# Optimization experiments

Hardware: AMD Instinct MI355X
Metric: run time of the kernel (lower is better)

The kernel has to match this reference:

```python
import jax, jax.numpy as jnp
import numpy as np

NUM_ACTIVE = 2  # num_active from init


def setup_inputs() -> dict:
    key = jax.random.key(0)
    k1, k2, k3, k4 = jax.random.split(key, 4)
    B, S, D, H, E = 2, 1024, 1024, 4096, 8
    x = jax.random.normal(k1, (B, S, D), jnp.float32)
    # router initialized to zeros in the torch module, but we use small random
    # weights so routing is non-degenerate for the correctness baseline
    router_w = jax.random.normal(k2, (D, E), jnp.float32) * 0.02
    router_b = jnp.zeros((E,), jnp.float32)
    w12 = jax.random.normal(k3, (E, D, 2 * H), jnp.float32) * (1.0 / np.sqrt(D))
    w3 = jax.random.normal(k4, (E, H, D), jnp.float32) * (1.0 / np.sqrt(H))
    return {"x": x, "router_w": router_w, "router_b": router_b, "w12": w12, "w3": w3}


def reference(x, router_w, router_b, w12, w3):
    E = router_w.shape[-1]
    # router (eval mode: no jitter noise)
    logits = x @ router_w + router_b                      # [B,S,E]
    scores = jax.nn.sigmoid(logits)
    top_s, top_i = jax.lax.top_k(scores, NUM_ACTIVE)      # [B,S,k]
    rw = top_s / (jnp.sum(top_s, axis=-1, keepdims=True) + 1e-6)
    # per-token combine weight for each expert: sum of routed slot weights
    cw = jnp.sum(jax.nn.one_hot(top_i, E, dtype=x.dtype) * rw[..., None], axis=-2)  # [B,S,E]
    # dense all-expert SwiGLU (same math as masked loop in the original)
    x12 = jnp.einsum('bsd,edh->ebsh', x, w12)             # [E,B,S,2H]
    x1, x2 = jnp.split(x12, 2, axis=-1)
    h = jax.nn.silu(x1) * x2                              # [E,B,S,H]
    out = jnp.einsum('ebsh,ehd,bse->bsd', h, w3, cw)      # [B,S,D]
    aux_loss = 0.01 * jnp.mean(logits ** 2)
    return out, aux_loss
```

## Files before the change

### kernel.cpp

```cpp
#include <hip/hip_runtime.h>
#include <hip/hip_bf16.h>

#define TOK 2048
#define DIM 1024
#define HID 4096
#define NE  8

typedef short bf16x8 __attribute__((ext_vector_type(8)));
typedef float f32x4 __attribute__((ext_vector_type(4)));
typedef unsigned short ushort_t;
typedef unsigned int uint_t;

#define SWZB(n) (((((n) >> 2) ^ ((n) >> 4)) & 3) << 4)

__device__ __forceinline__ ushort_t f2bf(float f) {
  uint_t b = __float_as_uint(f);
  uint_t r = (b + 0x7FFFu + ((b >> 16) & 1u)) >> 16;
  return (ushort_t)r;
}
__device__ __forceinline__ float bf2f(ushort_t u) {
  return __uint_as_float(((uint_t)u) << 16);
}
__device__ __forceinline__ uint_t pk2bf(float a, float b) {
  uint_t r;
  asm("v_cvt_pk_bf16_f32 %0, %1, %2" : "=v"(r) : "v"(a), "v"(b));
  return r;
}

__global__ void router_kernel(const float* __restrict__ x,
                              const float* __restrict__ rw,
                              const float* __restrict__ rb,
                              float* __restrict__ tok_ss,
                              int* __restrict__ top_e,
                              float* __restrict__ top_w,
                              ushort_t* __restrict__ xb) {
  const int t = blockIdx.x;
  const int lane = threadIdx.x;
  float acc[NE];
#pragma unroll
  for (int e = 0; e < NE; ++e) acc[e] = 0.f;
  const float4* x4 = (const float4*)(x + (size_t)t * DIM);
  uint2* xb2 = (uint2*)(xb + (size_t)t * DIM);
#pragma unroll
  for (int j = 0; j < 4; ++j) {
    int i = j * 64 + lane;
    float4 v = x4[i];
    uint2 u;
    u.x = pk2bf(v.x, v.y);
    u.y = pk2bf(v.z, v.w);
    xb2[i] = u;
    const float* w = rw + (size_t)i * 4 * NE;
    const float* vp = (const float*)&v;
#pragma unroll
    for (int c = 0; c < 4; ++c)
#pragma unroll
      for (int e = 0; e < NE; ++e) acc[e] += vp[c] * w[c * NE + e];
  }
#pragma unroll
  for (int e = 0; e < NE; ++e) {
    float v = acc[e];
#pragma unroll
    for (int off = 32; off > 0; off >>= 1) v += __shfl_down(v, off, 64);
    acc[e] = v;
  }
  if (lane == 0) {
    float sc[NE];
    float ss = 0.f;
#pragma unroll
    for (int e = 0; e < NE; ++e) {
      float lg = acc[e] + rb[e];
      ss += lg * lg;
      sc[e] = 1.f / (1.f + expf(-lg));
    }
    tok_ss[t] = ss;
    int i0 = 0;
#pragma unroll
    for (int e = 1; e < NE; ++e) if (sc[e] > sc[i0]) i0 = e;
    int i1 = (i0 == 0) ? 1 : 0;
#pragma unroll
    for (int e = 0; e < NE; ++e) if (e != i0 && sc[e] > sc[i1]) i1 = e;
    float s0 = sc[i0], s1 = sc[i1];
    float inv = 1.f / (s0 + s1 + 1e-6f);
    top_e[t * 2 + 0] = i0;
    top_e[t * 2 + 1] = i1;
    top_w[t * 2 + 0] = s0 * inv;
    top_w[t * 2 + 1] = s1 * inv;
  }
}

__global__ void scan_assign_kernel(const int* __restrict__ top_e,
                                   const float* __restrict__ top_w,
                                   int* __restrict__ offsets,
                                   int* __restrict__ list_tok,
                                   float* __restrict__ list_w) {
  __shared__ int lcount[NE];
  __shared__ int loff[NE + 1];
  __shared__ int lfill[NE];
  if (threadIdx.x < NE) lcount[threadIdx.x] = 0;
  __syncthreads();
  for (int i = threadIdx.x; i < TOK * 2; i += 256)
    atomicAdd(&lcount[top_e[i]], 1);
  __syncthreads();
  if (threadIdx.x == 0) {
    int o = 0;
    for (int e = 0; e < NE; ++e) { loff[e] = o; lfill[e] = o; o += lcount[e]; }
    loff[NE] = o;
  }
  __syncthreads();
  if (threadIdx.x <= NE) offsets[threadIdx.x] = loff[threadIdx.x];
  for (int i = threadIdx.x; i < TOK * 2; i += 256) {
    int e = top_e[i];
    int idx = atomicAdd(&lfill[e], 1);
    list_tok[idx] = i >> 1;
    list_w[idx] = top_w[i];
  }
}

__global__ void aux_kernel(const float* __restrict__ tok_ss, float* __restrict__ out_aux) {
  __shared__ float sm[256];
  float s = 0.f;
  for (int t = threadIdx.x; t < TOK; t += 256) s += tok_ss[t];
  sm[threadIdx.x] = s;
  __syncthreads();
  for (int w = 128; w > 0; w >>= 1) {
    if (threadIdx.x < w) sm[threadIdx.x] += sm[threadIdx.x + w];
    __syncthreads();
  }
  if (threadIdx.x == 0) *out_aux = 0.01f * sm[0] / (float)(TOK * NE);
}

__global__ __launch_bounds__(256)
void gemm1_mfma(const ushort_t* __restrict__ xb,
                const float* __restrict__ w12,
                const int* __restrict__ offsets, const int* __restrict__ list_tok,
                ushort_t* __restrict__ hhi) {
  __shared__ __align__(16) ushort_t Ah0[64 * 40];
  __shared__ __align__(16) ushort_t Ah1[64 * 40];
  __shared__ __align__(16) ushort_t B1h0[64 * 40];
  __shared__ __align__(16) ushort_t B1h1[64 * 40];
  __shared__ __align__(16) ushort_t B2h0[64 * 40];
  __shared__ __align__(16) ushort_t B2h1[64 * 40];

  const int e = blockIdx.y >> 5;
  const int rt = blockIdx.y & 31;
  const int rowstart = offsets[e] + rt * 64;
  const int rowend = offsets[e + 1];
  if (rowstart >= rowend) return;
  const int h0 = blockIdx.x * 64;
  const int tid = threadIdx.x;
  const int lane = tid & 63, wid = tid >> 6;
  const int wm = wid >> 1, wn = wid & 1;
  const int lr = lane & 15, kh = lane >> 4;

  f32x4 acc1[2][2], acc2[2][2];
#pragma unroll
  for (int mi = 0; mi < 2; ++mi)
#pragma unroll
    for (int nj = 0; nj < 2; ++nj) {
      acc1[mi][nj] = (f32x4){0.f, 0.f, 0.f, 0.f};
      acc2[mi][nj] = (f32x4){0.f, 0.f, 0.f, 0.f};
    }

  const int arow = tid >> 2, aseg = tid & 3;
  int ar = rowstart + arow;
  int atok = list_tok[ar < rowend ? ar : rowstart];
  const size_t asrc = (size_t)atok * DIM + aseg * 8;
  const int adst = arow * 40 + aseg * 8;

  const int p = tid >> 4, n4 = tid & 15;
  const float* w12e = w12 + (size_t)e * DIM * (2 * HID) + h0 + n4 * 4;
  char* B1c0 = (char*)B1h0;
  char* B1c1 = (char*)B1h1;
  char* B2c0 = (char*)B2h0;
  char* B2c1 = (char*)B2h1;

  int boff[2];
#pragma unroll
  for (int nj = 0; nj < 2; ++nj) {
    int n = wn * 32 + nj * 16 + lr;
    boff[nj] = n * 80 + ((kh * 16) ^ SWZB(n));
  }
  int bwoff[4];
#pragma unroll
  for (int c = 0; c < 4; ++c) {
    int n = n4 * 4 + c;
    bwoff[c] = n * 80 + ((4 * p) ^ SWZB(n));
  }

  uint4 ra0_0, ra1_0, ra0_1, ra1_1;
  float4 w1a0_0, w1b0_0, w2a0_0, w2b0_0, w1a1_0, w1b1_0, w2a1_0, w2b1_0;
  float4 w1a0_1, w1b0_1, w2a0_1, w2b0_1, w1a1_1, w1b1_1, w2a1_1, w2b1_1;

#define G1_LOAD(S, K0) do { \
    ra0_##S = *(const uint4*)&xb[asrc + (K0)]; \
    ra1_##S = *(const uint4*)&xb[asrc + (K0) + 32]; \
    const float* r0 = w12e + (size_t)((K0) + 2 * p) * (2 * HID); \
    w1a0_##S = *(const float4*)r0; \
    w1b0_##S = *(const float4*)(r0 + 2 * HID); \
    w2a0_##S = *(const float4*)(r0 + HID); \
    w2b0_##S = *(const float4*)(r0 + HID + 2 * HID); \
    const float* r1 = w12e + (size_t)((K0) + 32 + 2 * p) * (2 * HID); \
    w1a1_##S = *(const float4*)r1; \
    w1b1_##S = *(const float4*)(r1 + 2 * HID); \
    w2a1_##S = *(const float4*)(r1 + HID); \
    w2b1_##S = *(const float4*)(r1 + HID + 2 * HID); \
  } while (0)

#define G1_STORE(S) do { \
    *(uint4*)&Ah0[adst] = ra0_##S; \
    *(uint4*)&Ah1[adst] = ra1_##S; \
    const float* p1a0 = (const float*)&w1a0_##S; \
    const float* p1b0 = (const float*)&w1b0_##S; \
    const float* p2a0 = (const float*)&w2a0_##S; \
    const float* p2b0 = (const float*)&w2b0_##S; \
    const float* p1a1 = (const float*)&w1a1_##S; \
    const float* p1b1 = (const float*)&w1b1_##S; \
    const float* p2a1 = (const float*)&w2a1_##S; \
    const float* p2b1 = (const float*)&w2b1_##S; \
    _Pragma("unroll") \
    for (int c = 0; c < 4; ++c) { \
      *(uint_t*)(B1c0 + bwoff[c]) = pk2bf(p1a0[c], p1b0[c]); \
      *(uint_t*)(B2c0 + bwoff[c]) = pk2bf(p2a0[c], p2b0[c]); \
      *(uint_t*)(B1c1 + bwoff[c]) = pk2bf(p1a1[c], p1b1[c]); \
      *(uint_t*)(B2c1 + bwoff[c]) = pk2bf(p2a1[c], p2b1[c]); \
    } } while (0)

#define G1_COMPUTE() do { \
    { \
      bf16x8 af[2], b1f[2], b2f[2]; \
      _Pragma("unroll") \
      for (int mi = 0; mi < 2; ++mi) \
        af[mi] = *(bf16x8*)&Ah0[(wm * 32 + mi * 16 + lr) * 40 + kh * 8]; \
      _Pragma("unroll") \
      for (int nj = 0; nj < 2; ++nj) { \
        b1f[nj] = *(bf16x8*)(B1c0 + boff[nj]); \
        b2f[nj] = *(bf16x8*)(B2c0 + boff[nj]); \
      } \
      _Pragma("unroll") \
      for (int mi = 0; mi < 2; ++mi) \
        _Pragma("unroll") \
        for (int nj = 0; nj < 2; ++nj) { \
          acc1[mi][nj] = __builtin_amdgcn_mfma_f32_16x16x32_bf16(af[mi], b1f[nj], acc1[mi][nj], 0, 0, 0); \
          acc2[mi][nj] = __builtin_amdgcn_mfma_f32_16x16x32_bf16(af[mi], b2f[nj], acc2[mi][nj], 0, 0, 0); \
        } \
    } \
    { \
      bf16x8 af[2], b1f[2], b2f[2]; \
      _Pragma("unroll") \
      for (int mi = 0; mi < 2; ++mi) \
        af[mi] = *(bf16x8*)&Ah1[(wm * 32 + mi * 16 + lr) * 40 + kh * 8]; \
      _Pragma("unroll") \
      for (int nj = 0; nj < 2; ++nj) { \
        b1f[nj] = *(bf16x8*)(B1c1 + boff[nj]); \
        b2f[nj] = *(bf16x8*)(B2c1 + boff[nj]); \
      } \
      _Pragma("unroll") \
      for (int mi = 0; mi < 2; ++mi) \
        _Pragma("unroll") \
        for (int nj = 0; nj < 2; ++nj) { \
          acc1[mi][nj] = __builtin_amdgcn_mfma_f32_16x16x32_bf16(af[mi], b1f[nj], acc1[mi][nj], 0, 0, 0); \
          acc2[mi][nj] = __builtin_amdgcn_mfma_f32_16x16x32_bf16(af[mi], b2f[nj], acc2[mi][nj], 0, 0, 0); \
        } \
    } } while (0)

  G1_LOAD(0, 0);
  G1_LOAD(1, 64);
#pragma unroll 1
  for (int k0 = 0; k0 < DIM; k0 += 128) {
    G1_STORE(0);
    __syncthreads();
    if (k0 + 128 < DIM) G1_LOAD(0, k0 + 128);
    G1_COMPUTE();
    __syncthreads();
    G1_STORE(1);
    __syncthreads();
    if (k0 + 192 < DIM) G1_LOAD(1, k0 + 192);
    G1_COMPUTE();
    __syncthreads();
  }
#undef G1_LOAD
#undef G1_STORE
#undef G1_COMPUTE

#pragma unroll
  for (int mi = 0; mi < 2; ++mi)
#pragma unroll
    for (int nj = 0; nj < 2; ++nj)
#pragma unroll
      for (int r = 0; r < 4; ++r) {
        int row_t = wm * 32 + mi * 16 + kh * 4 + r;
        int gr = rowstart + row_t;
        if (gr < rowend) {
          int col = h0 + wn * 32 + nj * 16 + lr;
          float v1 = acc1[mi][nj][r], v2 = acc2[mi][nj][r];
          float hv = (v1 / (1.f + expf(-v1))) * v2;
          hhi[(size_t)gr * HID + col] = f2bf(hv);
        }
      }
}

__global__ __launch_bounds__(256)
void gemm2_mfma(const ushort_t* __restrict__ hhi,
                const float* __restrict__ w3,
                const int* __restrict__ offsets, const float* __restrict__ list_w,
                const int* __restrict__ list_tok,
                float* __restrict__ out) {
  __shared__ __align__(16) ushort_t As0[64 * 40];
  __shared__ __align__(16) ushort_t As1[64 * 40];
  __shared__ __align__(16) ushort_t Bs0[64 * 40];
  __shared__ __align__(16) ushort_t Bs1[64 * 40];

  const int e = blockIdx.y >> 4;
  const int rt = blockIdx.y & 15;
  const int rowstart = offsets[e] + rt * 64;
  const int rowend = offsets[e + 1];
  if (rowstart >= rowend) return;
  const int d0 = blockIdx.x * 64;
  const int tid = threadIdx.x;
  const int lane = tid & 63, wid = tid >> 6;
  const int wm = wid >> 1, wn = wid & 1;
  const int lr = lane & 15, kh = lane >> 4;

  f32x4 acc[2][2];
#pragma unroll
  for (int mi = 0; mi < 2; ++mi)
#pragma unroll
    for (int nj = 0; nj < 2; ++nj) acc[mi][nj] = (f32x4){0.f, 0.f, 0.f, 0.f};

  const int arow = tid >> 2, aseg = tid & 3;
  int gr = rowstart + arow; if (gr >= rowend) gr = rowstart;
  const size_t asrc = (size_t)gr * HID + aseg * 8;
  const int adst = arow * 40 + aseg * 8;

  const int p = tid >> 4, n4 = tid & 15;
  const float* w3e = w3 + (size_t)e * HID * DIM + d0 + n4 * 4;
  char* Bs0c = (char*)Bs0;
  char* Bs1c = (char*)Bs1;

  int boff[2];
#pragma unroll
  for (int nj = 0; nj < 2; ++nj) {
    int n = wn * 32 + nj * 16 + lr;
    boff[nj] = n * 80 + ((kh * 16) ^ SWZB(n));
  }
  int bwoff[4];
#pragma unroll
  for (int c = 0; c < 4; ++c) {
    int n = n4 * 4 + c;
    bwoff[c] = n * 80 + ((4 * p) ^ SWZB(n));
  }

  uint4 ra0_0, ra1_0, ra0_1, ra1_1;
  float4 rb00_0, rb01_0, rb10_0, rb11_0;
  float4 rb00_1, rb01_1, rb10_1, rb11_1;

#define G2_LOAD(S, K0) do { \
    ra0_##S = *(const uint4*)&hhi[asrc + (K0)]; \
    ra1_##S = *(const uint4*)&hhi[asrc + (K0) + 32]; \
    const float* r0 = w3e + (size_t)((K0) + 2 * p) * DIM; \
    rb00_##S = *(const float4*)r0; \
    rb01_##S = *(const float4*)(r0 + DIM); \
    const float* r1 = w3e + (size_t)((K0) + 32 + 2 * p) * DIM; \
    rb10_##S = *(const float4*)r1; \
    rb11_##S = *(const float4*)(r1 + DIM); \
  } while (0)

#define G2_STORE(S) do { \
    *(uint4*)&As0[adst] = ra0_##S; \
    *(uint4*)&As1[adst] = ra1_##S; \
    const float* pv0 = (const float*)&rb00_##S; \
    const float* pv1 = (const float*)&rb01_##S; \
    const float* pw0 = (const float*)&rb10_##S; \
    const float* pw1 = (const float*)&rb11_##S; \
    _Pragma("unroll") \
    for (int c = 0; c < 4; ++c) { \
      *(uint_t*)(Bs0c + bwoff[c]) = pk2bf(pv0[c], pv1[c]); \
      *(uint_t*)(Bs1c + bwoff[c]) = pk2bf(pw0[c], pw1[c]); \
    } } while (0)

#define G2_COMPUTE() do { \
    { \
      bf16x8 af[2], bf[2]; \
      _Pragma("unroll") \
      for (int mi = 0; mi < 2; ++mi) \
        af[mi] = *(bf16x8*)&As0[(wm * 32 + mi * 16 + lr) * 40 + kh * 8]; \
      _Pragma("unroll") \
      for (int nj = 0; nj < 2; ++nj) \
        bf[nj] = *(bf16x8*)(Bs0c + boff[nj]); \
      _Pragma("unroll") \
      for (int mi = 0; mi < 2; ++mi) \
        _Pragma("unroll") \
        for (int nj = 0; nj < 2; ++nj) \
          acc[mi][nj] = __builtin_amdgcn_mfma_f32_16x16x32_bf16(af[mi], bf[nj], acc[mi][nj], 0, 0, 0); \
    } \
    { \
      bf16x8 af[2], bf[2]; \
      _Pragma("unroll") \
      for (int mi = 0; mi < 2; ++mi) \
        af[mi] = *(bf16x8*)&As1[(wm * 32 + mi * 16 + lr) * 40 + kh * 8]; \
      _Pragma("unroll") \
      for (int nj = 0; nj < 2; ++nj) \
        bf[nj] = *(bf16x8*)(Bs1c + boff[nj]); \
      _Pragma("unroll") \
      for (int mi = 0; mi < 2; ++mi) \
        _Pragma("unroll") \
        for (int nj = 0; nj < 2; ++nj) \
          acc[mi][nj] = __builtin_amdgcn_mfma_f32_16x16x32_bf16(af[mi], bf[nj], acc[mi][nj], 0, 0, 0); \
    } } while (0)

  G2_LOAD(0, 0);
  G2_LOAD(1, 64);
#pragma unroll 1
  for (int k0 = 0; k0 < HID; k0 += 128) {
    G2_STORE(0);
    __syncthreads();
    if (k0 + 128 < HID) G2_LOAD(0, k0 + 128);
    G2_COMPUTE();
    __syncthreads();
    G2_STORE(1);
    __syncthreads();
    if (k0 + 192 < HID) G2_LOAD(1, k0 + 192);
    G2_COMPUTE();
    __syncthreads();
  }
#undef G2_LOAD
#undef G2_STORE
#undef G2_COMPUTE

#pragma unroll
  for (int mi = 0; mi < 2; ++mi)
#pragma unroll
    for (int nj = 0; nj < 2; ++nj)
#pragma unroll
      for (int r = 0; r < 4; ++r) {
        int grr = rowstart + wm * 32 + mi * 16 + kh * 4 + r;
        if (grr < rowend) {
          int col = d0 + wn * 32 + nj * 16 + lr;
          int tok = list_tok[grr];
          atomicAdd(&out[(size_t)tok * DIM + col], acc[mi][nj][r] * list_w[grr]);
        }
      }
}

extern "C" void kernel_launch(void* const* d_in, const int* in_sizes, int n_in,
                              void* d_out, int out_size, void* d_ws, size_t ws_size,
                              hipStream_t stream) {
  const float* x   = (const float*)d_in[0];
  const float* rw  = (const float*)d_in[1];
  const float* rb  = (const float*)d_in[2];
  const float* w12 = (const float*)d_in[3];
  const float* w3  = (const float*)d_in[4];
  float* out = (float*)d_out;

  char* ws = (char*)d_ws;
  size_t off = 0;
  auto alloc = [&](size_t bytes) {
    void* p = ws + off;
    off = (off + bytes + 255) & ~255ULL;
    return p;
  };
  int*   offsets  = (int*)alloc((NE + 1) * 4);
  float* tok_ss   = (float*)alloc(TOK * 4);
  int*   top_e    = (int*)alloc(TOK * 2 * 4);
  float* top_w    = (float*)alloc(TOK * 2 * 4);
  int*   list_tok = (int*)alloc(TOK * 2 * 4);
  float* list_w   = (float*)alloc(TOK * 2 * 4);

  ushort_t* xb  = (ushort_t*)alloc((size_t)TOK * DIM * 2);
  ushort_t* hhi = (ushort_t*)alloc((size_t)TOK * 2 * HID * 2);

  hipMemsetAsync(out, 0, (size_t)TOK * DIM * 4, stream);

  hipLaunchKernelGGL(router_kernel, dim3(TOK), dim3(64), 0, stream,
                     x, rw, rb, tok_ss, top_e, top_w, xb);
  hipLaunchKernelGGL(scan_assign_kernel, dim3(1), dim3(256), 0, stream,
                     top_e, top_w, offsets, list_tok, list_w);
  hipLaunchKernelGGL(aux_kernel, dim3(1), dim3(256), 0, stream,
                     tok_ss, out + (size_t)TOK * DIM);

  hipLaunchKernelGGL(gemm1_mfma, dim3(HID / 64, NE * 32), dim3(256), 0, stream,
                     xb, w12, offsets, list_tok, hhi);
  hipLaunchKernelGGL(gemm2_mfma, dim3(DIM / 64, NE * 16), dim3(256), 0, stream,
                     hhi, w3, offsets, list_w, list_tok, out);
}
```

Measured before the change: 364.0 us.

## Load A fragments straight from global into registers and double gemm1 row tile

Both MoE GEMMs stop staging the gathered activation tile in shared memory. Each lane now loads its MFMA A fragments directly from global memory into registers, so only the fp32-to-bf16 weight tile goes through LDS. gemm1 grows its row tile from 64 to 128 tokens per block, which halves how often each block re-reads and converts the fp32 w12 weights, and its K step shrinks to 32 with a single weight buffer. gemm2's grid is widened to 64 row tiles per expert so experts holding more than 1024 routed rows are fully covered; the extra blocks mostly exit early. The trade-off is less-coalesced 16-byte direct global loads, more registers per thread and more barriers per K stride in gemm1.

```diff
diff --git a/kernel.cpp b/kernel.cpp
--- a/kernel.cpp
+++ b/kernel.cpp
@@ -134,16 +134,12 @@
                 const float* __restrict__ w12,
                 const int* __restrict__ offsets, const int* __restrict__ list_tok,
                 ushort_t* __restrict__ hhi) {
-  __shared__ __align__(16) ushort_t Ah0[64 * 40];
-  __shared__ __align__(16) ushort_t Ah1[64 * 40];
-  __shared__ __align__(16) ushort_t B1h0[64 * 40];
-  __shared__ __align__(16) ushort_t B1h1[64 * 40];
-  __shared__ __align__(16) ushort_t B2h0[64 * 40];
-  __shared__ __align__(16) ushort_t B2h1[64 * 40];
+  __shared__ __align__(16) ushort_t B1[64 * 40];
+  __shared__ __align__(16) ushort_t B2[64 * 40];
 
   const int e = blockIdx.y >> 5;
   const int rt = blockIdx.y & 31;
-  const int rowstart = offsets[e] + rt * 64;
+  const int rowstart = offsets[e] + rt * 128;
   const int rowend = offsets[e + 1];
   if (rowstart >= rowend) return;
   const int h0 = blockIdx.x * 64;
@@ -152,27 +148,27 @@
   const int wm = wid >> 1, wn = wid & 1;
   const int lr = lane & 15, kh = lane >> 4;
 
-  f32x4 acc1[2][2], acc2[2][2];
-#pragma unroll
-  for (int mi = 0; mi < 2; ++mi)
+  f32x4 acc1[4][2], acc2[4][2];
+#pragma unroll
+  for (int mi = 0; mi < 4; ++mi)
 #pragma unroll
     for (int nj = 0; nj < 2; ++nj) {
       acc1[mi][nj] = (f32x4){0.f, 0.f, 0.f, 0.f};
       acc2[mi][nj] = (f32x4){0.f, 0.f, 0.f, 0.f};
     }
 
-  const int arow = tid >> 2, aseg = tid & 3;
-  int ar = rowstart + arow;
-  int atok = list_tok[ar < rowend ? ar : rowstart];
-  const size_t asrc = (size_t)atok * DIM + aseg * 8;
-  const int adst = arow * 40 + aseg * 8;
+  const ushort_t* aP[4];
+#pragma unroll
+  for (int mi = 0; mi < 4; ++mi) {
+    int r = rowstart + wm * 64 + mi * 16 + lr;
+    int rr = (r < rowend) ? r : rowstart;
+    aP[mi] = xb + (size_t)list_tok[rr] * DIM + kh * 8;
+  }
 
   const int p = tid >> 4, n4 = tid & 15;
   const float* w12e = w12 + (size_t)e * DIM * (2 * HID) + h0 + n4 * 4;
-  char* B1c0 = (char*)B1h0;
-  char* B1c1 = (char*)B1h1;
-  char* B2c0 = (char*)B2h0;
-  char* B2c1 = (char*)B2h1;
+  char* B1c = (char*)B1;
+  char* B2c = (char*)B2;
 
   int boff[2];
 #pragma unroll
@@ -187,108 +183,79 @@
     bwoff[c] = n * 80 + ((4 * p) ^ SWZB(n));
   }
 
-  uint4 ra0_0, ra1_0, ra0_1, ra1_1;
-  float4 w1a0_0, w1b0_0, w2a0_0, w2b0_0, w1a1_0, w1b1_0, w2a1_0, w2b1_0;
-  float4 w1a0_1, w1b0_1, w2a0_1, w2b0_1, w1a1_1, w1b1_1, w2a1_1, w2b1_1;
-
-#define G1_LOAD(S, K0) do { \
-    ra0_##S = *(const uint4*)&xb[asrc + (K0)]; \
-    ra1_##S = *(const uint4*)&xb[asrc + (K0) + 32]; \
+  bf16x8 a0[4], a1[4];
+  float4 w1a, w1b, w2a, w2b;
+
+#define G1_ALOAD(SET, K0) do { \
+    _Pragma("unroll") \
+    for (int mi = 0; mi < 4; ++mi) SET[mi] = *(const bf16x8*)(aP[mi] + (K0)); \
+  } while (0)
+
+#define G1_BLOAD(K0) do { \
     const float* r0 = w12e + (size_t)((K0) + 2 * p) * (2 * HID); \
-    w1a0_##S = *(const float4*)r0; \
-    w1b0_##S = *(const float4*)(r0 + 2 * HID); \
-    w2a0_##S = *(const float4*)(r0 + HID); \
-    w2b0_##S = *(const float4*)(r0 + HID + 2 * HID); \
-    const float* r1 = w12e + (size_t)((K0) + 32 + 2 * p) * (2 * HID); \
-    w1a1_##S = *(const float4*)r1; \
-    w1b1_##S = *(const float4*)(r1 + 2 * HID); \
-    w2a1_##S = *(const float4*)(r1 + HID); \
-    w2b1_##S = *(const float4*)(r1 + HID + 2 * HID); \
+    w1a = *(const float4*)r0; \
+    w1b = *(const float4*)(r0 + 2 * HID); \
+    w2a = *(const float4*)(r0 + HID); \
+    w2b = *(const float4*)(r0 + HID + 2 * HID); \
   } while (0)
 
-#define G1_STORE(S) do { \
-    *(uint4*)&Ah0[adst] = ra0_##S; \
-    *(uint4*)&Ah1[adst] = ra1_##S; \
-    const float* p1a0 = (const float*)&w1a0_##S; \
-    const float* p1b0 = (const float*)&w1b0_##S; \
-    const float* p2a0 = (const float*)&w2a0_##S; \
-    const float* p2b0 = (const float*)&w2b0_##S; \
-    const float* p1a1 = (const float*)&w1a1_##S; \
-    const float* p1b1 = (const float*)&w1b1_##S; \
-    const float* p2a1 = (const float*)&w2a1_##S; \
-    const float* p2b1 = (const float*)&w2b1_##S; \
+#define G1_BSTORE() do { \
+    const float* p1a = (const float*)&w1a; \
+    const float* p1b = (const float*)&w1b; \
+    const float* p2a = (const float*)&w2a; \
+    const float* p2b = (const float*)&w2b; \
     _Pragma("unroll") \
     for (int c = 0; c < 4; ++c) { \
-      *(uint_t*)(B1c0 + bwoff[c]) = pk2bf(p1a0[c], p1b0[c]); \
-      *(uint_t*)(B2c0 + bwoff[c]) = pk2bf(p2a0[c], p2b0[c]); \
-      *(uint_t*)(B1c1 + bwoff[c]) = pk2bf(p1a1[c], p1b1[c]); \
-      *(uint_t*)(B2c1 + bwoff[c]) = pk2bf(p2a1[c], p2b1[c]); \
+      *(uint_t*)(B1c + bwoff[c]) = pk2bf(p1a[c], p1b[c]); \
+      *(uint_t*)(B2c + bwoff[c]) = pk2bf(p2a[c], p2b[c]); \
     } } while (0)
 
-#define G1_COMPUTE() do { \
-    { \
-      bf16x8 af[2], b1f[2], b2f[2]; \
-      _Pragma("unroll") \
-      for (int mi = 0; mi < 2; ++mi) \
-        af[mi] = *(bf16x8*)&Ah0[(wm * 32 + mi * 16 + lr) * 40 + kh * 8]; \
+#define G1_MFMA(ASET) do { \
+    bf16x8 b1f[2], b2f[2]; \
+    _Pragma("unroll") \
+    for (int nj = 0; nj < 2; ++nj) { \
+      b1f[nj] = *(bf16x8*)(B1c + boff[nj]); \
+      b2f[nj] = *(bf16x8*)(B2c + boff[nj]); \
+    } \
+    _Pragma("unroll") \
+    for (int mi = 0; mi < 4; ++mi) \
       _Pragma("unroll") \
       for (int nj = 0; nj < 2; ++nj) { \
-        b1f[nj] = *(bf16x8*)(B1c0 + boff[nj]); \
-        b2f[nj] = *(bf16x8*)(B2c0 + boff[nj]); \
-      } \
-      _Pragma("unroll") \
-      for (int mi = 0; mi < 2; ++mi) \
-        _Pragma("unroll") \
-        for (int nj = 0; nj < 2; ++nj) { \
-          acc1[mi][nj] = __builtin_amdgcn_mfma_f32_16x16x32_bf16(af[mi], b1f[nj], acc1[mi][nj], 0, 0, 0); \
-          acc2[mi][nj] = __builtin_amdgcn_mfma_f32_16x16x32_bf16(af[mi], b2f[nj], acc2[mi][nj], 0, 0, 0); \
-        } \
-    } \
-    { \
-      bf16x8 af[2], b1f[2], b2f[2]; \
-      _Pragma("unroll") \
-      for (int mi = 0; mi < 2; ++mi) \
-        af[mi] = *(bf16x8*)&Ah1[(wm * 32 + mi * 16 + lr) * 40 + kh * 8]; \
-      _Pragma("unroll") \
-      for (int nj = 0; nj < 2; ++nj) { \
-        b1f[nj] = *(bf16x8*)(B1c1 + boff[nj]); \
-        b2f[nj] = *(bf16x8*)(B2c1 + boff[nj]); \
-      } \
-      _Pragma("unroll") \
-      for (int mi = 0; mi < 2; ++mi) \
-        _Pragma("unroll") \
-        for (int nj = 0; nj < 2; ++nj) { \
-          acc1[mi][nj] = __builtin_amdgcn_mfma_f32_16x16x32_bf16(af[mi], b1f[nj], acc1[mi][nj], 0, 0, 0); \
-          acc2[mi][nj] = __builtin_amdgcn_mfma_f32_16x16x32_bf16(af[mi], b2f[nj], acc2[mi][nj], 0, 0, 0); \
-        } \
-    } } while (0)
-
-  G1_LOAD(0, 0);
-  G1_LOAD(1, 64);
+        acc1[mi][nj] = __builtin_amdgcn_mfma_f32_16x16x32_bf16(ASET[mi], b1f[nj], acc1[mi][nj], 0, 0, 0); \
+        acc2[mi][nj] = __builtin_amdgcn_mfma_f32_16x16x32_bf16(ASET[mi], b2f[nj], acc2[mi][nj], 0, 0, 0); \
+      } } while (0)
+
+  G1_ALOAD(a0, 0);
+  G1_BLOAD(0);
 #pragma unroll 1
-  for (int k0 = 0; k0 < DIM; k0 += 128) {
-    G1_STORE(0);
-    __syncthreads();
-    if (k0 + 128 < DIM) G1_LOAD(0, k0 + 128);
-    G1_COMPUTE();
-    __syncthreads();
-    G1_STORE(1);
-    __syncthreads();
-    if (k0 + 192 < DIM) G1_LOAD(1, k0 + 192);
-    G1_COMPUTE();
-    __syncthreads();
-  }
-#undef G1_LOAD
-#undef G1_STORE
-#undef G1_COMPUTE
-
-#pragma unroll
-  for (int mi = 0; mi < 2; ++mi)
+  for (int k0 = 0; k0 < DIM; k0 += 64) {
+    G1_BSTORE();
+    __syncthreads();
+    G1_BLOAD(k0 + 32);
+    G1_ALOAD(a1, k0 + 32);
+    G1_MFMA(a0);
+    __syncthreads();
+    G1_BSTORE();
+    __syncthreads();
+    if (k0 + 64 < DIM) {
+      G1_BLOAD(k0 + 64);
+      G1_ALOAD(a0, k0 + 64);
+    }
+    G1_MFMA(a1);
+    __syncthreads();
+  }
+#undef G1_ALOAD
+#undef G1_BLOAD
+#undef G1_BSTORE
+#undef G1_MFMA
+
+#pragma unroll
+  for (int mi = 0; mi < 4; ++mi)
 #pragma unroll
     for (int nj = 0; nj < 2; ++nj)
 #pragma unroll
       for (int r = 0; r < 4; ++r) {
-        int row_t = wm * 32 + mi * 16 + kh * 4 + r;
+        int row_t = wm * 64 + mi * 16 + kh * 4 + r;
         int gr = rowstart + row_t;
         if (gr < rowend) {
           int col = h0 + wn * 32 + nj * 16 + lr;
@@ -305,13 +272,11 @@
                 const int* __restrict__ offsets, const float* __restrict__ list_w,
                 const int* __restrict__ list_tok,
                 float* __restrict__ out) {
-  __shared__ __align__(16) ushort_t As0[64 * 40];
-  __shared__ __align__(16) ushort_t As1[64 * 40];
   __shared__ __align__(16) ushort_t Bs0[64 * 40];
   __shared__ __align__(16) ushort_t Bs1[64 * 40];
 
-  const int e = blockIdx.y >> 4;
-  const int rt = blockIdx.y & 15;
+  const int e = blockIdx.y >> 6;
+  const int rt = blockIdx.y & 63;
   const int rowstart = offsets[e] + rt * 64;
   const int rowend = offsets[e + 1];
   if (rowstart >= rowend) return;
@@ -327,10 +292,13 @@
 #pragma unroll
     for (int nj = 0; nj < 2; ++nj) acc[mi][nj] = (f32x4){0.f, 0.f, 0.f, 0.f};
 
-  const int arow = tid >> 2, aseg = tid & 3;
-  int gr = rowstart + arow; if (gr >= rowend) gr = rowstart;
-  const size_t asrc = (size_t)gr * HID + aseg * 8;
-  const int adst = arow * 40 + aseg * 8;
+  const ushort_t* aP[2];
+#pragma unroll
+  for (int mi = 0; mi < 2; ++mi) {
+    int r = rowstart + wm * 32 + mi * 16 + lr;
+    int rr = (r < rowend) ? r : rowstart;
+    aP[mi] = hhi + (size_t)rr * HID + kh * 8;
+  }
 
   const int p = tid >> 4, n4 = tid & 15;
   const float* w3e = w3 + (size_t)e * HID * DIM + d0 + n4 * 4;
@@ -350,81 +318,80 @@
     bwoff[c] = n * 80 + ((4 * p) ^ SWZB(n));
   }
 
-  uint4 ra0_0, ra1_0, ra0_1, ra1_1;
-  float4 rb00_0, rb01_0, rb10_0, rb11_0;
-  float4 rb00_1, rb01_1, rb10_1, rb11_1;
-
-#define G2_LOAD(S, K0) do { \
-    ra0_##S = *(const uint4*)&hhi[asrc + (K0)]; \
-    ra1_##S = *(const uint4*)&hhi[asrc + (K0) + 32]; \
+  bf16x8 sa0[4], sa1[4];
+  float4 rb00, rb01, rb10, rb11;
+
+#define G2_ALOAD(SET, K0) do { \
+    _Pragma("unroll") \
+    for (int mi = 0; mi < 2; ++mi) { \
+      SET[mi]     = *(const bf16x8*)(aP[mi] + (K0)); \
+      SET[2 + mi] = *(const bf16x8*)(aP[mi] + (K0) + 32); \
+    } } while (0)
+
+#define G2_BLOAD(K0) do { \
     const float* r0 = w3e + (size_t)((K0) + 2 * p) * DIM; \
-    rb00_##S = *(const float4*)r0; \
-    rb01_##S = *(const float4*)(r0 + DIM); \
+    rb00 = *(const float4*)r0; \
+    rb01 = *(const float4*)(r0 + DIM); \
     const float* r1 = w3e + (size_t)((K0) + 32 + 2 * p) * DIM; \
-    rb10_##S = *(const float4*)r1; \
-    rb11_##S = *(const float4*)(r1 + DIM); \
+    rb10 = *(const float4*)r1; \
+    rb11 = *(const float4*)(r1 + DIM); \
   } while (0)
 
-#define G2_STORE(S) do { \
-    *(uint4*)&As0[adst] = ra0_##S; \
-    *(uint4*)&As1[adst] = ra1_##S; \
-    const float* pv0 = (const float*)&rb00_##S; \
-    const float* pv1 = (const float*)&rb01_##S; \
-    const float* pw0 = (const float*)&rb10_##S; \
-    const float* pw1 = (const float*)&rb11_##S; \
+#define G2_BSTORE() do { \
+    const float* pv0 = (const float*)&rb00; \
+    const float* pv1 = (const float*)&rb01; \
+    const float* pw0 = (const float*)&rb10; \
+    const float* pw1 = (const float*)&rb11; \
     _Pragma("unroll") \
     for (int c = 0; c < 4; ++c) { \
       *(uint_t*)(Bs0c + bwoff[c]) = pk2bf(pv0[c], pv1[c]); \
       *(uint_t*)(Bs1c + bwoff[c]) = pk2bf(pw0[c], pw1[c]); \
     } } while (0)
 
-#define G2_COMPUTE() do { \
+#define G2_COMPUTE(SET) do { \
     { \
-      bf16x8 af[2], bf[2]; \
+      bf16x8 bf[2]; \
       _Pragma("unroll") \
-      for (int mi = 0; mi < 2; ++mi) \
-        af[mi] = *(bf16x8*)&As0[(wm * 32 + mi * 16 + lr) * 40 + kh * 8]; \
-      _Pragma("unroll") \
-      for (int nj = 0; nj < 2; ++nj) \
-        bf[nj] = *(bf16x8*)(Bs0c + boff[nj]); \
+      for (int nj = 0; nj < 2; ++nj) bf[nj] = *(bf16x8*)(Bs0c + boff[nj]); \
       _Pragma("unroll") \
       for (int mi = 0; mi < 2; ++mi) \
         _Pragma("unroll") \
         for (int nj = 0; nj < 2; ++nj) \
-          acc[mi][nj] = __builtin_amdgcn_mfma_f32_16x16x32_bf16(af[mi], bf[nj], acc[mi][nj], 0, 0, 0); \
+          acc[mi][nj] = __builtin_amdgcn_mfma_f32_16x16x32_bf16(SET[mi], bf[nj], acc[mi][nj], 0, 0, 0); \
     } \
     { \
-      bf16x8 af[2], bf[2]; \
+      bf16x8 bf[2]; \
       _Pragma("unroll") \
-      for (int mi = 0; mi < 2; ++mi) \
-        af[mi] = *(bf16x8*)&As1[(wm * 32 + mi * 16 + lr) * 40 + kh * 8]; \
-      _Pragma("unroll") \
-      for (int nj = 0; nj < 2; ++nj) \
-        bf[nj] = *(bf16x8*)(Bs1c + boff[nj]); \
+      for (int nj = 0; nj < 2; ++nj) bf[nj] = *(bf16x8*)(Bs1c + boff[nj]); \
       _Pragma("unroll") \
       for (int mi = 0; mi < 2; ++mi) \
         _Pragma("unroll") \
         for (int nj = 0; nj < 2; ++nj) \
-          acc[mi][nj] = __builtin_amdgcn_mfma_f32_16x16x32_bf16(af[mi], bf[nj], acc[mi][nj], 0, 0, 0); \
+          acc[mi][nj] = __builtin_amdgcn_mfma_f32_16x16x32_bf16(SET[2 + mi], bf[nj], acc[mi][nj], 0, 0, 0); \
     } } while (0)
 
-  G2_LOAD(0, 0);
-  G2_LOAD(1, 64);
+  G2_ALOAD(sa0, 0);
+  G2_BLOAD(0);
 #pragma unroll 1
   for (int k0 = 0; k0 < HID; k0 += 128) {
-    G2_STORE(0);
-    __syncthreads();
-    if (k0 + 128 < HID) G2_LOAD(0, k0 + 128);
-    G2_COMPUTE();
-    __syncthreads();
-    G2_STORE(1);
-    __syncthreads();
-    if (k0 + 192 < HID) G2_LOAD(1, k0 + 192);
-    G2_COMPUTE();
-    __syncthreads();
-  }
-#undef G2_LOAD
-#undef G2_STORE
+    G2_BSTORE();
+    __syncthreads();
+    G2_BLOAD(k0 + 64);
+    G2_ALOAD(sa1, k0 + 64);
+    G2_COMPUTE(sa0);
+    __syncthreads();
+    G2_BSTORE();
+    __syncthreads();
+    if (k0 + 128 < HID) {
+      G2_BLOAD(k0 + 128);
+      G2_ALOAD(sa0, k0 + 128);
+    }
+    G2_COMPUTE(sa1);
+    __syncthreads();
+  }
+#undef G2_ALOAD
+#undef G2_BLOAD
+#undef G2_BSTORE
 #undef G2_COMPUTE
 
 #pragma unroll
@@ -480,6 +447,6 @@
 
   hipLaunchKernelGGL(gemm1_mfma, dim3(HID / 64, NE * 32), dim3(256), 0, stream,
                      xb, w12, offsets, list_tok, hhi);
-  hipLaunchKernelGGL(gemm2_mfma, dim3(DIM / 64, NE * 16), dim3(256), 0, stream,
+  hipLaunchKernelGGL(gemm2_mfma, dim3(DIM / 64, NE * 64), dim3(256), 0, stream,
                      hhi, w3, offsets, list_w, list_tok, out);
 }
```

Result: slower. 477.1 us (+31.1%).
